# Optimization experiments

Measured on AMD Instinct MI355X. Metric: run time of the kernel, lower is better.

Reference implementation:

```python
import jax, jax.numpy as jnp
import numpy as np

IN_FEATURES = 4096
OUT_FEATURES = 8192
GROUP_SIZE = 16
NUM_GROUPS = IN_FEATURES * OUT_FEATURES // GROUP_SIZE  # 2_097_152


def block_dequantize_2bit(packed, normalization):
    # packed: [G, group_size//4] int32 holding uint8 values; norm: [G, 1] fp16
    shifts = jnp.arange(4, dtype=packed.dtype) * 2  # bit offsets 0,2,4,6
    # unpacked column 4k+i comes from packed column k, bits 2i..2i+1
    u = ((packed[:, :, None] >> shifts) & 3).astype(jnp.float32)  # [G, gs/4, 4]
    u = u.reshape(packed.shape[0], -1)  # [G, group_size]
    norm = normalization.astype(jnp.float32)
    return (u / 3.0) * (2.0 * norm) - norm  # [G, group_size]


def setup_inputs() -> dict:
    key = jax.random.key(0)
    k_x, k_q, k_n, k_b = jax.random.split(key, 4)
    x = jax.random.normal(k_x, (256, IN_FEATURES), dtype=jnp.float32)
    # packed 2-bit weights: random bytes (store as int32 for clean bit ops in jax)
    weight_q2 = jax.random.randint(k_q, (NUM_GROUPS, GROUP_SIZE // 4), 0, 256, dtype=jnp.int32)
    # per-group normalization (abs-max), positive, fp16 as in the module buffer
    weight_norm = (jax.random.uniform(k_n, (NUM_GROUPS, 1), dtype=jnp.float32) * 0.05 + 1e-4).astype(jnp.float16)
    bias = jax.random.normal(k_b, (OUT_FEATURES,), dtype=jnp.float32) * 0.01
    return {"x": x, "weight_q2": weight_q2, "weight_norm": weight_norm, "bias": bias}


def reference(x, weight_q2, weight_norm, bias):
    weight = block_dequantize_2bit(weight_q2, weight_norm).reshape(OUT_FEATURES, IN_FEATURES)
    return jnp.dot(x.astype(jnp.float32), weight.T) + bias
```

## Files before the change

### kernel.cpp

```cpp
#include <hip/hip_runtime.h>
#include <hip/hip_fp16.h>

#define IN_F   4096
#define OUT_F  8192
#define M_ROWS 256

#define SPLITK  8
#define KSTEPS  (IN_F / 32)
#define NIT     (KSTEPS / SPLITK)
#define NSTRIPS (OUT_F / 64)

typedef __attribute__((ext_vector_type(8))) short  short8;
typedef __attribute__((ext_vector_type(4))) float  float4v;

union pk8 { uint4 u; short8 s; };
union hbits { __half h; unsigned short u; };

__device__ inline unsigned int pack_bf16(float lo, float hi) {
    return __builtin_amdgcn_perm(__float_as_uint(hi), __float_as_uint(lo), 0x07060302u);
}

__device__ inline float h2f_bits(unsigned int b) {
    hbits t; t.u = (unsigned short)b;
    return __half2float(t.h);
}

__global__ void cvt_x_kernel(const float* __restrict__ x, uint4* __restrict__ xb) {
    const int tid = blockIdx.x * blockDim.x + threadIdx.x;
    if (tid >= (M_ROWS * IN_F) / 8) return;
    const int lane = tid & 63;
    const int mf   = (tid >> 6) & 15;
    const int ks   = tid >> 10;
    const int m    = mf * 16 + (lane & 15);
    const int k    = ks * 32 + (lane >> 4) * 8;
    const float* p = x + m * IN_F + k;
    float4 v0 = ((const float4*)p)[0], v1 = ((const float4*)p)[1];
    uint4 o;
    o.x = pack_bf16(v0.x, v0.y); o.y = pack_bf16(v0.z, v0.w);
    o.z = pack_bf16(v1.x, v1.y); o.w = pack_bf16(v1.z, v1.w);
    xb[tid] = o;
}

__global__ void init_out_kernel(const float* __restrict__ bias, float* __restrict__ out) {
    int i = blockIdx.x * blockDim.x + threadIdx.x;
    if (i < (M_ROWS * OUT_F) / 4) {
        float4 b = ((const float4*)bias)[i & (OUT_F / 4 - 1)];
        ((float4*)out)[i] = b;
    }
}

__global__ void reduce_out_kernel(const float4* __restrict__ P,
                                  const float* __restrict__ bias,
                                  float4* __restrict__ out, int splitk) {
    const int i = blockIdx.x * blockDim.x + threadIdx.x;
    if (i >= (M_ROWS * OUT_F) / 4) return;
    float4 s = P[i];
    for (int z = 1; z < splitk; ++z) {
        float4 p = P[(size_t)z * (M_ROWS * OUT_F / 4) + i];
        s.x += p.x; s.y += p.y; s.z += p.z; s.w += p.w;
    }
    float4 b = ((const float4*)bias)[i & (OUT_F / 4 - 1)];
    s.x += b.x; s.y += b.y; s.z += b.z; s.w += b.w;
    out[i] = s;
}

__global__ __launch_bounds__(256) void repack_w_kernel(
    const int* __restrict__ wq, const void* __restrict__ wnorm,
    uint4* __restrict__ bs) {
    __shared__ unsigned int qlds[64 * 64];
    __shared__ unsigned int nlds[64 * 32];

    const int t = threadIdx.x;
    const int s = blockIdx.x;
    const int w = blockIdx.y;

    const float cand0 = *(const float*)wnorm;
    const bool  nf32  = (cand0 > 1e-5f && cand0 < 0.1f);

    {
        const int p    = t & 63;
        const int rsub = t >> 6;
#pragma unroll
        for (int j = 0; j < 16; ++j) {
            const int row  = j * 4 + rsub;
            const int rowg = s * 64 + row;
            int4 d = *(const int4*)(wq + (size_t)rowg * (IN_F / 4) + w * 256 + p * 4);
            unsigned int t01   = __builtin_amdgcn_perm((unsigned)d.y, (unsigned)d.x, 0x00000400u);
            unsigned int t23   = __builtin_amdgcn_perm((unsigned)d.w, (unsigned)d.z, 0x00000400u);
            unsigned int bytes = __builtin_amdgcn_perm(t23, t01, 0x05040100u);
            const int chunk = (p >> 1) ^ (row & 31);
            qlds[row * 64 + ((chunk << 1) | (p & 1))] = bytes;
        }
    }
    {
        const int p    = t & 31;
        const int rsub = t >> 5;
#pragma unroll
        for (int j = 0; j < 8; ++j) {
            const int row  = j * 8 + rsub;
            const int rowg = s * 64 + row;
            unsigned int packed;
            if (nf32) {
                const float2 v = *(const float2*)((const float*)wnorm +
                                   (size_t)rowg * (IN_F / 16) + w * 64 + p * 2);
                hbits a, b; a.h = __float2half(v.x); b.h = __float2half(v.y);
                packed = (unsigned int)a.u | ((unsigned int)b.u << 16);
            } else {
                packed = *(const unsigned int*)((const unsigned short*)wnorm +
                           (size_t)rowg * (IN_F / 16) + w * 64 + p * 2);
            }
            nlds[row * 32 + (p ^ (row & 31))] = packed;
        }
    }
    __syncthreads();

    const int base = (s * KSTEPS + w * 32) * 64;
#pragma unroll
    for (int e = 0; e < 8; ++e) {
        const int id   = e * 256 + t;
        const int ks   = id >> 6;
        const int lane = id & 63;
        const int quad = lane >> 4;
        const int l15  = lane & 15;
        const int q2   = quad >> 1;
        const int hsel = quad & 1;
        unsigned int q16[4], n16[4];
#pragma unroll
        for (int j = 0; j < 4; ++j) {
            const int row = j * 16 + l15;
            const int cs  = ks ^ (row & 31);
            const unsigned int qv = qlds[row * 64 + ((cs << 1) | q2)];
            q16[j] = (qv >> (hsel * 16)) & 0xFFFFu;
            const unsigned int nv = nlds[row * 32 + cs];
            n16[j] = (nv >> (q2 * 16)) & 0xFFFFu;
        }
        uint4 r;
        r.x = q16[0] | (q16[1] << 16);
        r.y = q16[2] | (q16[3] << 16);
        r.z = n16[0] | (n16[1] << 16);
        r.w = n16[2] | (n16[3] << 16);
        bs[base + id] = r;
    }
}

template <bool XB, bool BS, bool PW>
__global__ __launch_bounds__(512, 2) void gemm2bit_kernel(
    const float* __restrict__ xf,
    const uint4* __restrict__ xb,
    const uint4* __restrict__ bs,
    const int*   __restrict__ wq,
    const void*  __restrict__ wnorm,
    float*       __restrict__ out)
{
    const int t    = threadIdx.x;
    const int wave = t >> 6;
    const int lane = t & 63;
    const int l15  = lane & 15;
    const int quad = lane >> 4;
    const int wm   = wave >> 2;
    const int wn   = wave & 3;

    const int s0   = blockIdx.x * 8 + wn * 2;
    const int m0   = blockIdx.y * 128 + wm * 64;
    const int mb   = blockIdx.y * 8 + wm * 4;
    const int ks0  = blockIdx.z * NIT;

    bool nf32 = false;
    if (!BS) {
        const float cand0 = *(const float*)wnorm;
        nf32 = (cand0 > 1e-5f && cand0 < 0.1f);
    }

    float4v acc[4][8] = {};

    auto loadA = [&](uint4 (&a)[4], int ks) {
        if (XB) {
#pragma unroll
            for (int i = 0; i < 4; ++i)
                a[i] = xb[(size_t)(ks * 16 + mb + i) * 64 + lane];
        } else {
#pragma unroll
            for (int i = 0; i < 4; ++i) {
                const float* p = xf + (size_t)(m0 + i * 16 + l15) * IN_F + ks * 32 + quad * 8;
                float4 v0 = ((const float4*)p)[0], v1 = ((const float4*)p)[1];
                a[i].x = pack_bf16(v0.x, v0.y); a[i].y = pack_bf16(v0.z, v0.w);
                a[i].z = pack_bf16(v1.x, v1.y); a[i].w = pack_bf16(v1.z, v1.w);
            }
        }
    };

    auto loadB1 = [&](uint4& bv, int strip, int ks) {
        if (BS) {
            bv = bs[(size_t)(strip * KSTEPS + ks) * 64 + lane];
        } else {
            unsigned int q16[4], n16[4];
#pragma unroll
            for (int j = 0; j < 4; ++j) {
                const int n = strip * 64 + j * 16 + l15;
                const int2 q = *(const int2*)((const char*)wq +
                                  (size_t)n * (IN_F / 4) * 4 + (size_t)ks * 32 + quad * 8);
                q16[j] = (unsigned int)((q.x & 0xFF) | ((q.y & 0xFF) << 8));
                const int g = n * (IN_F / 16) + ks * 2 + (quad >> 1);
                if (nf32) {
                    hbits h; h.h = __float2half(((const float*)wnorm)[g]);
                    n16[j] = h.u;
                } else {
                    n16[j] = ((const unsigned short*)wnorm)[g];
                }
            }
            bv.x = q16[0] | (q16[1] << 16);
            bv.y = q16[2] | (q16[3] << 16);
            bv.z = n16[0] | (n16[1] << 16);
            bv.w = n16[2] | (n16[3] << 16);
        }
    };

    auto procRec = [&](uint4 (&a)[4], const uint4& bv, int jb) {
        const unsigned int qd[2] = { bv.x, bv.y };
        const unsigned int nd[2] = { bv.z, bv.w };
#pragma unroll
        for (int j = 0; j < 4; ++j) {
            const unsigned int qn = (qd[j >> 1] >> ((j & 1) * 16)) & 0xFFFFu;
            const float nC = h2f_bits((nd[j >> 1] >> ((j & 1) * 16)) & 0xFFFFu);
            const float s  = nC * (2.0f / 3.0f);
            float f[8];
#pragma unroll
            for (int i = 0; i < 4; ++i)
                f[i]     = fmaf((float)((qn >> (2 * i)) & 3), s, -nC);
#pragma unroll
            for (int i = 0; i < 4; ++i)
                f[4 + i] = fmaf((float)((qn >> (8 + 2 * i)) & 3), s, -nC);
            pk8 b;
            b.u.x = pack_bf16(f[0], f[1]); b.u.y = pack_bf16(f[2], f[3]);
            b.u.z = pack_bf16(f[4], f[5]); b.u.w = pack_bf16(f[6], f[7]);
#pragma unroll
            for (int i = 0; i < 4; ++i) {
                pk8 av; av.u = a[i];
                acc[i][jb + j] = __builtin_amdgcn_mfma_f32_16x16x32_bf16(av.s, b.s, acc[i][jb + j], 0, 0, 0);
            }
        }
    };

    uint4 a0[4], a1[4], b0[2], b1[2];
    loadA(a0, ks0);     loadB1(b0[0], s0, ks0);     loadB1(b0[1], s0 + 1, ks0);
    loadA(a1, ks0 + 1); loadB1(b1[0], s0, ks0 + 1); loadB1(b1[1], s0 + 1, ks0 + 1);

    for (int it = 0; it < NIT; it += 2) {
        procRec(a0, b0[0], 0); procRec(a0, b0[1], 4);
        if (it + 2 < NIT) {
            const int ks = ks0 + it + 2;
            loadA(a0, ks); loadB1(b0[0], s0, ks); loadB1(b0[1], s0 + 1, ks);
        }
        procRec(a1, b1[0], 0); procRec(a1, b1[1], 4);
        if (it + 3 < NIT) {
            const int ks = ks0 + it + 3;
            loadA(a1, ks); loadB1(b1[0], s0, ks); loadB1(b1[1], s0 + 1, ks);
        }
    }

    if (PW) {
        float* P = out + (size_t)blockIdx.z * (M_ROWS * OUT_F);
#pragma unroll
        for (int j = 0; j < 8; ++j) {
            const int col = s0 * 64 + (j >> 2) * 64 + (j & 3) * 16 + l15;
#pragma unroll
            for (int i = 0; i < 4; ++i) {
                const int row0 = m0 + i * 16 + quad * 4;
#pragma unroll
                for (int r = 0; r < 4; ++r)
                    P[(size_t)(row0 + r) * OUT_F + col] = acc[i][j][r];
            }
        }
    } else {
#pragma unroll
        for (int j = 0; j < 8; ++j) {
            const int col = s0 * 64 + (j >> 2) * 64 + (j & 3) * 16 + l15;
#pragma unroll
            for (int i = 0; i < 4; ++i) {
                const int row0 = m0 + i * 16 + quad * 4;
#pragma unroll
                for (int r = 0; r < 4; ++r)
                    atomicAdd(&out[(size_t)(row0 + r) * OUT_F + col], acc[i][j][r]);
            }
        }
    }
}

extern "C" void kernel_launch(void* const* d_in, const int* in_sizes, int n_in,
                              void* d_out, int out_size, void* d_ws, size_t ws_size,
                              hipStream_t stream) {
    const float* x    = (const float*)d_in[0];
    const int*   wq   = (const int*)d_in[1];
    const void*  wn   = (const void*)d_in[2];
    const float* bias = (const float*)d_in[3];
    float*       out  = (float*)d_out;

    const size_t xb_bytes = (size_t)M_ROWS * IN_F * 2;
    const size_t bs_bytes = (size_t)NSTRIPS * KSTEPS * 64 * 16;
    const size_t pw_bytes = (size_t)SPLITK * M_ROWS * OUT_F * 4;

    dim3 grid(OUT_F / 512, M_ROWS / 128, SPLITK);

    if (ws_size >= xb_bytes + bs_bytes + pw_bytes) {
        uint4* xbv = (uint4*)d_ws;
        uint4* bsw = (uint4*)((char*)d_ws + xb_bytes);
        float* pw  = (float*)((char*)d_ws + xb_bytes + bs_bytes);
        cvt_x_kernel<<<dim3((M_ROWS * IN_F / 8) / 256), 256, 0, stream>>>(x, xbv);
        repack_w_kernel<<<dim3(NSTRIPS, KSTEPS / 32), 256, 0, stream>>>(wq, wn, bsw);
        gemm2bit_kernel<true, true, true><<<grid, 512, 0, stream>>>(
            nullptr, xbv, bsw, wq, wn, pw);
        reduce_out_kernel<<<dim3((M_ROWS * OUT_F / 4) / 256), 256, 0, stream>>>(
            (const float4*)pw, bias, (float4*)out, SPLITK);
    } else if (ws_size >= xb_bytes + bs_bytes) {
        uint4* xbv = (uint4*)d_ws;
        uint4* bsw = (uint4*)((char*)d_ws + xb_bytes);
        init_out_kernel<<<dim3((M_ROWS * OUT_F / 4) / 256), 256, 0, stream>>>(bias, out);
        cvt_x_kernel<<<dim3((M_ROWS * IN_F / 8) / 256), 256, 0, stream>>>(x, xbv);
        repack_w_kernel<<<dim3(NSTRIPS, KSTEPS / 32), 256, 0, stream>>>(wq, wn, bsw);
        gemm2bit_kernel<true, true, false><<<grid, 512, 0, stream>>>(
            nullptr, xbv, bsw, wq, wn, out);
    } else if (ws_size >= xb_bytes) {
        uint4* xbv = (uint4*)d_ws;
        init_out_kernel<<<dim3((M_ROWS * OUT_F / 4) / 256), 256, 0, stream>>>(bias, out);
        cvt_x_kernel<<<dim3((M_ROWS * IN_F / 8) / 256), 256, 0, stream>>>(x, xbv);
        gemm2bit_kernel<true, false, false><<<grid, 512, 0, stream>>>(
            nullptr, xbv, nullptr, wq, wn, out);
    } else {
        init_out_kernel<<<dim3((M_ROWS * OUT_F / 4) / 256), 256, 0, stream>>>(bias, out);
        gemm2bit_kernel<false, false, false><<<grid, 512, 0, stream>>>(
            x, nullptr, nullptr, wq, wn, out);
    }
}
```

Measured before the change: 139.3 us.

## Merge x conversion into weight repack kernel and deepen B prefetch

Folds the fp32-to-bf16 conversion of x into the weight repack launch as an extra grid row, which removes one kernel launch. The GEMM main loop now keeps B fragments in a four-deep rotating register buffer instead of two and is fully unrolled, so weight loads are issued further ahead of use. The split-K reduction loop is unrolled with a compile-time count. The deeper buffer and full unroll raise register pressure, which could lower occupancy.

```diff
diff --git a/kernel.cpp b/kernel.cpp
--- a/kernel.cpp
+++ b/kernel.cpp
@@ -23,6 +23,14 @@
 __device__ inline float h2f_bits(unsigned int b) {
     hbits t; t.u = (unsigned short)b;
     return __half2float(t.h);
+}
+
+__global__ void init_out_kernel(const float* __restrict__ bias, float* __restrict__ out) {
+    int i = blockIdx.x * blockDim.x + threadIdx.x;
+    if (i < (M_ROWS * OUT_F) / 4) {
+        float4 b = ((const float4*)bias)[i & (OUT_F / 4 - 1)];
+        ((float4*)out)[i] = b;
+    }
 }
 
 __global__ void cvt_x_kernel(const float* __restrict__ x, uint4* __restrict__ xb) {
@@ -41,21 +49,14 @@
     xb[tid] = o;
 }
 
-__global__ void init_out_kernel(const float* __restrict__ bias, float* __restrict__ out) {
-    int i = blockIdx.x * blockDim.x + threadIdx.x;
-    if (i < (M_ROWS * OUT_F) / 4) {
-        float4 b = ((const float4*)bias)[i & (OUT_F / 4 - 1)];
-        ((float4*)out)[i] = b;
-    }
-}
-
 __global__ void reduce_out_kernel(const float4* __restrict__ P,
                                   const float* __restrict__ bias,
-                                  float4* __restrict__ out, int splitk) {
+                                  float4* __restrict__ out) {
     const int i = blockIdx.x * blockDim.x + threadIdx.x;
     if (i >= (M_ROWS * OUT_F) / 4) return;
     float4 s = P[i];
-    for (int z = 1; z < splitk; ++z) {
+#pragma unroll
+    for (int z = 1; z < SPLITK; ++z) {
         float4 p = P[(size_t)z * (M_ROWS * OUT_F / 4) + i];
         s.x += p.x; s.y += p.y; s.z += p.z; s.w += p.w;
     }
@@ -64,15 +65,35 @@
     out[i] = s;
 }
 
-__global__ __launch_bounds__(256) void repack_w_kernel(
+__global__ __launch_bounds__(256) void prep_kernel(
     const int* __restrict__ wq, const void* __restrict__ wnorm,
-    uint4* __restrict__ bs) {
+    uint4* __restrict__ bs, const float* __restrict__ x,
+    uint4* __restrict__ xb) {
     __shared__ unsigned int qlds[64 * 64];
     __shared__ unsigned int nlds[64 * 32];
 
     const int t = threadIdx.x;
     const int s = blockIdx.x;
     const int w = blockIdx.y;
+
+    if (w == 4) {
+#pragma unroll
+        for (int e = 0; e < 4; ++e) {
+            const int tid = e * (NSTRIPS * 256) + s * 256 + t;
+            const int lane = tid & 63;
+            const int mf   = (tid >> 6) & 15;
+            const int ks   = tid >> 10;
+            const int m    = mf * 16 + (lane & 15);
+            const int k    = ks * 32 + (lane >> 4) * 8;
+            const float* p = x + (size_t)m * IN_F + k;
+            float4 v0 = ((const float4*)p)[0], v1 = ((const float4*)p)[1];
+            uint4 o;
+            o.x = pack_bf16(v0.x, v0.y); o.y = pack_bf16(v0.z, v0.w);
+            o.z = pack_bf16(v1.x, v1.y); o.w = pack_bf16(v1.z, v1.w);
+            xb[tid] = o;
+        }
+        return;
+    }
 
     const float cand0 = *(const float*)wnorm;
     const bool  nf32  = (cand0 > 1e-5f && cand0 < 0.1f);
@@ -241,20 +262,27 @@
         }
     };
 
-    uint4 a0[4], a1[4], b0[2], b1[2];
-    loadA(a0, ks0);     loadB1(b0[0], s0, ks0);     loadB1(b0[1], s0 + 1, ks0);
-    loadA(a1, ks0 + 1); loadB1(b1[0], s0, ks0 + 1); loadB1(b1[1], s0 + 1, ks0 + 1);
-
+    uint4 a0[4], a1[4], bb[4][2];
+    loadA(a0, ks0); loadA(a1, ks0 + 1);
+#pragma unroll
+    for (int d = 0; d < 4; ++d) {
+        loadB1(bb[d][0], s0, ks0 + d);
+        loadB1(bb[d][1], s0 + 1, ks0 + d);
+    }
+
+#pragma unroll
     for (int it = 0; it < NIT; it += 2) {
-        procRec(a0, b0[0], 0); procRec(a0, b0[1], 4);
-        if (it + 2 < NIT) {
-            const int ks = ks0 + it + 2;
-            loadA(a0, ks); loadB1(b0[0], s0, ks); loadB1(b0[1], s0 + 1, ks);
-        }
-        procRec(a1, b1[0], 0); procRec(a1, b1[1], 4);
-        if (it + 3 < NIT) {
-            const int ks = ks0 + it + 3;
-            loadA(a1, ks); loadB1(b1[0], s0, ks); loadB1(b1[1], s0 + 1, ks);
+        procRec(a0, bb[it & 3][0], 0); procRec(a0, bb[it & 3][1], 4);
+        if (it + 2 < NIT) loadA(a0, ks0 + it + 2);
+        if (it + 4 < NIT) {
+            loadB1(bb[it & 3][0], s0, ks0 + it + 4);
+            loadB1(bb[it & 3][1], s0 + 1, ks0 + it + 4);
+        }
+        procRec(a1, bb[(it + 1) & 3][0], 0); procRec(a1, bb[(it + 1) & 3][1], 4);
+        if (it + 3 < NIT) loadA(a1, ks0 + it + 3);
+        if (it + 5 < NIT) {
+            loadB1(bb[(it + 1) & 3][0], s0, ks0 + it + 5);
+            loadB1(bb[(it + 1) & 3][1], s0 + 1, ks0 + it + 5);
         }
     }
 
@@ -305,18 +333,16 @@
         uint4* xbv = (uint4*)d_ws;
         uint4* bsw = (uint4*)((char*)d_ws + xb_bytes);
         float* pw  = (float*)((char*)d_ws + xb_bytes + bs_bytes);
-        cvt_x_kernel<<<dim3((M_ROWS * IN_F / 8) / 256), 256, 0, stream>>>(x, xbv);
-        repack_w_kernel<<<dim3(NSTRIPS, KSTEPS / 32), 256, 0, stream>>>(wq, wn, bsw);
+        prep_kernel<<<dim3(NSTRIPS, 5), 256, 0, stream>>>(wq, wn, bsw, x, xbv);
         gemm2bit_kernel<true, true, true><<<grid, 512, 0, stream>>>(
             nullptr, xbv, bsw, wq, wn, pw);
         reduce_out_kernel<<<dim3((M_ROWS * OUT_F / 4) / 256), 256, 0, stream>>>(
-            (const float4*)pw, bias, (float4*)out, SPLITK);
+            (const float4*)pw, bias, (float4*)out);
     } else if (ws_size >= xb_bytes + bs_bytes) {
         uint4* xbv = (uint4*)d_ws;
         uint4* bsw = (uint4*)((char*)d_ws + xb_bytes);
         init_out_kernel<<<dim3((M_ROWS * OUT_F / 4) / 256), 256, 0, stream>>>(bias, out);
-        cvt_x_kernel<<<dim3((M_ROWS * IN_F / 8) / 256), 256, 0, stream>>>(x, xbv);
-        repack_w_kernel<<<dim3(NSTRIPS, KSTEPS / 32), 256, 0, stream>>>(wq, wn, bsw);
+        prep_kernel<<<dim3(NSTRIPS, 5), 256, 0, stream>>>(wq, wn, bsw, x, xbv);
         gemm2bit_kernel<true, true, false><<<grid, 512, 0, stream>>>(
             nullptr, xbv, bsw, wq, wn, out);
     } else if (ws_size >= xb_bytes) {
```

After: 137.9 us. About the same (-1.0%).
